# Kernel tuning notes

Measured on AMD Instinct MI355X. Metric: run time of the kernel, lower is better.

## Reference

```python
import jax, jax.numpy as jnp
import numpy as np

EMBED_DIM = 1024
NUM_HEADS = 16
HEAD_DIM = EMBED_DIM // NUM_HEADS
SCALE = 1.0 / np.sqrt(HEAD_DIM).astype(np.float32)


def setup_inputs() -> dict:
    key = jax.random.key(0)
    ks = jax.random.split(key, 9)
    B, T, C = 2, 2048, EMBED_DIM
    s = 1.0 / np.sqrt(C).astype(np.float32)  # torch Linear init scale (approx, uniform bound)
    return {
        "x_q": jax.random.normal(ks[0], (B, T, C), dtype=jnp.float32),
        "attn_mask": jnp.zeros((T, T), dtype=jnp.float32),
        "Wq": jax.random.uniform(ks[1], (C, C), jnp.float32, -s, s),
        "bq": jax.random.uniform(ks[2], (C,), jnp.float32, -s, s),
        "Wk": jax.random.uniform(ks[3], (C, C), jnp.float32, -s, s),
        "bk": jax.random.uniform(ks[4], (C,), jnp.float32, -s, s),
        "Wv": jax.random.uniform(ks[5], (C, C), jnp.float32, -s, s),
        "bv": jax.random.uniform(ks[6], (C,), jnp.float32, -s, s),
        "Wo": jax.random.uniform(ks[7], (C, C), jnp.float32, -s, s),
        "bo": jax.random.uniform(ks[8], (C,), jnp.float32, -s, s),
    }


def reference(x_q, attn_mask, Wq, bq, Wk, bk, Wv, bv, Wo, bo):
    B, Tq, C = x_q.shape
    # self-attention: x_kv = x_q
    q = (x_q @ Wq.T + bq).reshape(B, Tq, NUM_HEADS, HEAD_DIM)
    k = (x_q @ Wk.T + bk).reshape(B, Tq, NUM_HEADS, HEAD_DIM)
    v = (x_q @ Wv.T + bv).reshape(B, Tq, NUM_HEADS, HEAD_DIM)
    # (B, H, Tq, Tk)
    scores = jnp.einsum('bqhd,bkhd->bhqk', q, k) * SCALE
    scores = scores + attn_mask[None, None, :, :]  # 2D additive mask path
    attn = jax.nn.softmax(scores, axis=-1)  # dropout p=0.0 -> identity
    out = jnp.einsum('bhqk,bkhd->bqhd', attn, v).reshape(B, Tq, C)
    out = out @ Wo.T + bo
    return out
```

## Files before the change

kernel.cpp:

```cpp
#include <hip/hip_runtime.h>
#include <hip/hip_bf16.h>
#include <stdint.h>

typedef _Float16 f16x8_t __attribute__((ext_vector_type(8)));
typedef _Float16 f16x4_t __attribute__((ext_vector_type(4)));
typedef float    f32x4_t __attribute__((ext_vector_type(4)));

#define T_SEQ 2048
#define NH    16
#define HD    64
#define CDIM  1024
#define NTOK  4096
#define QSCALE 0.18033688011112042f
#define LOG2E  1.4426950408889634f

__device__ __forceinline__ void async_ld16(void* lds, const void* g) {
    __builtin_amdgcn_global_load_lds(
        (const __attribute__((address_space(1))) uint32_t*)g,
        (__attribute__((address_space(3))) uint32_t*)lds, 16, 0, 0);
}

__global__ __launch_bounds__(256)
void prep_all(const float* __restrict__ x, const float* __restrict__ Wq,
              const float* __restrict__ Wk, const float* __restrict__ Wv,
              const float* __restrict__ Wo, const float* __restrict__ mask,
              _Float16* __restrict__ xh, _Float16* __restrict__ Wqkvh,
              _Float16* __restrict__ Woh, int* __restrict__ flag)
{
    const int XQ = NTOK * CDIM / 4;
    const int WQ = CDIM * CDIM / 4;
    int i = blockIdx.x * 256 + threadIdx.x;
    if (i < XQ + 4 * WQ) {
        const float* s; _Float16* d; int off;
        if (i < XQ) { s = x; d = xh; off = i; }
        else {
            int j = i - XQ; int w = j >> 18; off = j & (WQ - 1);
            s = (w == 0) ? Wq : (w == 1) ? Wk : (w == 2) ? Wv : Wo;
            d = (w == 3) ? Woh : Wqkvh + (size_t)w * CDIM * CDIM;
        }
        float4 v = ((const float4*)s)[off];
        f16x4_t h = {(_Float16)v.x, (_Float16)v.y, (_Float16)v.z, (_Float16)v.w};
        ((f16x4_t*)d)[off] = h;
    } else {
        int off = i - (XQ + 4 * WQ);
        float4 v = ((const float4*)mask)[off];
        if (v.x != 0.f || v.y != 0.f || v.z != 0.f || v.w != 0.f) atomicOr(flag, 1);
    }
}

template<int MODE>
__global__ __launch_bounds__(256)
void gemm_f16(const _Float16* __restrict__ Ag, const _Float16* __restrict__ Bg,
              const float* __restrict__ b0, const float* __restrict__ b1,
              const float* __restrict__ b2,
              _Float16* __restrict__ Qo, _Float16* __restrict__ Ko,
              _Float16* __restrict__ Vto, float* __restrict__ Fo)
{
    __shared__ _Float16 sA[3][128 * 32];
    __shared__ _Float16 sB[3][128 * 32];
    const int K = CDIM;
    const int tid  = threadIdx.x;
    const int lane = tid & 63, wv = tid >> 6;
    const int wr = wv >> 1, wc = wv & 1;
    const int bid = blockIdx.x;
    const int xcd = bid & 7, L = bid >> 3;
    const int sb = L & 31, st = L >> 5;
    const int rowA0 = (st * 8 + (sb & 7)) * 128;
    const int rowB0 = (xcd * 4 + (sb >> 3)) * 128;
    const int srow = lane >> 2;
    const int scol = (((lane & 3) ^ (srow & 3)) * 8);
    const int fr = lane & 15, fg = lane >> 4;
    const int rsw = (fg ^ (fr & 3)) * 8;
    f32x4_t acc[4][4] = {};

#define STAGE(buf, kk) do {                                                     \
        _Pragma("unroll")                                                       \
        for (int i_ = 0; i_ < 2; ++i_) {                                        \
            const int eoff = i_ * 2048 + wv * 512;                              \
            const int r_ = i_ * 64 + wv * 16 + srow;                            \
            async_ld16(&sA[buf][eoff], Ag + (size_t)(rowA0 + r_) * K + (kk) + scol); \
            async_ld16(&sB[buf][eoff], Bg + (size_t)(rowB0 + r_) * K + (kk) + scol); \
        } } while (0)

    STAGE(0, 0);
    int cur = 0;
    for (int k0 = 0; k0 < K; k0 += 32) {
        const int nxt = (cur == 2) ? 0 : cur + 1;
        if (k0 + 32 < K) {
            STAGE(nxt, k0 + 32);
            asm volatile("s_waitcnt vmcnt(4)" ::: "memory");
        } else {
            asm volatile("s_waitcnt vmcnt(0)" ::: "memory");
        }
        __builtin_amdgcn_s_barrier();
        __builtin_amdgcn_sched_barrier(0);
        f16x8_t a[4], b[4];
#pragma unroll
        for (int mi = 0; mi < 4; ++mi)
            a[mi] = *(const f16x8_t*)&sA[cur][(wr * 64 + mi * 16 + fr) * 32 + rsw];
#pragma unroll
        for (int ni = 0; ni < 4; ++ni)
            b[ni] = *(const f16x8_t*)&sB[cur][(wc * 64 + ni * 16 + fr) * 32 + rsw];
#pragma unroll
        for (int mi = 0; mi < 4; ++mi)
#pragma unroll
            for (int ni = 0; ni < 4; ++ni)
                acc[mi][ni] = __builtin_amdgcn_mfma_f32_16x16x32_f16(a[mi], b[ni], acc[mi][ni], 0, 0, 0);
        cur = nxt;
    }
#undef STAGE

    if (MODE == 0) {
        const int which = rowA0 >> 10;
        const float* bp = (which == 0) ? b0 : ((which == 1) ? b1 : b2);
#pragma unroll
        for (int mi = 0; mi < 4; ++mi) {
            const int cc = (rowA0 & 1023) + wr * 64 + mi * 16 + fg * 4;
            const float4 bv = *(const float4*)&bp[cc];
            const int h = cc >> 6, d0 = cc & 63;
#pragma unroll
            for (int ni = 0; ni < 4; ++ni) {
                const int tok = rowB0 + wc * 64 + ni * 16 + fr;
                const int bh = (tok >> 11) * NH + h, tt = tok & (T_SEQ - 1);
                const float v0 = acc[mi][ni][0] + bv.x, v1 = acc[mi][ni][1] + bv.y;
                const float v2 = acc[mi][ni][2] + bv.z, v3 = acc[mi][ni][3] + bv.w;
                if (which == 0) {
                    f16x4_t hq = {(_Float16)(v0 * QSCALE), (_Float16)(v1 * QSCALE),
                                  (_Float16)(v2 * QSCALE), (_Float16)(v3 * QSCALE)};
                    *(f16x4_t*)&Qo[((size_t)bh * T_SEQ + tt) * HD + d0] = hq;
                } else if (which == 1) {
                    f16x4_t hk = {(_Float16)v0, (_Float16)v1, (_Float16)v2, (_Float16)v3};
                    *(f16x4_t*)&Ko[((size_t)bh * 32 + (tt >> 6)) * 4096 +
                                   (d0 >> 3) * 512 + (tt & 63) * 8 + (d0 & 7)] = hk;
                } else {
                    const size_t vb_ = ((size_t)bh * 32 + (tt >> 6)) * 4096 +
                                       (size_t)((tt >> 3) & 7) * 512 + (tt & 7);
                    Vto[vb_ + (d0 + 0) * 8] = (_Float16)v0;
                    Vto[vb_ + (d0 + 1) * 8] = (_Float16)v1;
                    Vto[vb_ + (d0 + 2) * 8] = (_Float16)v2;
                    Vto[vb_ + (d0 + 3) * 8] = (_Float16)v3;
                }
            }
        }
    } else {
#pragma unroll
        for (int mi = 0; mi < 4; ++mi) {
            const int cc = rowA0 + wr * 64 + mi * 16 + fg * 4;
            const float4 bv = *(const float4*)&b0[cc];
#pragma unroll
            for (int ni = 0; ni < 4; ++ni) {
                const int tok = rowB0 + wc * 64 + ni * 16 + fr;
                float4 ov = {acc[mi][ni][0] + bv.x, acc[mi][ni][1] + bv.y,
                             acc[mi][ni][2] + bv.z, acc[mi][ni][3] + bv.w};
                *(float4*)&Fo[(size_t)tok * CDIM + cc] = ov;
            }
        }
    }
}

__global__ __launch_bounds__(512, 4)
void attn_f16(const _Float16* __restrict__ Q, const _Float16* __restrict__ Kc,
              const _Float16* __restrict__ Vc, const float* __restrict__ mask,
              const int* __restrict__ mflag, _Float16* __restrict__ AO)
{
    __shared__ __align__(16) _Float16 sK[3][4096];
    __shared__ __align__(16) _Float16 sV[3][4096];

    const int tid = threadIdx.x;
    const int lane = tid & 63, wv = tid >> 6;
    const int fr = lane & 15, fg = lane >> 4;
    const int bid = blockIdx.x;
    const int swz = (bid & 7) * 64 + (bid >> 3);
    const int qx = swz & 15, bh = swz >> 4;
    const int b = bh >> 4, h = bh & (NH - 1);
    const int q0 = qx * 128 + wv * 16;
    const _Float16* Qb  = Q  + (size_t)bh * T_SEQ * HD;
    const _Float16* Kbh = Kc + (size_t)bh * (T_SEQ * HD);
    const _Float16* Vbh = Vc + (size_t)bh * (T_SEQ * HD);
    const int soff = wv * 512 + lane * 8;

    f16x8_t qf[2];
#pragma unroll
    for (int dc = 0; dc < 2; ++dc)
        qf[dc] = *(const f16x8_t*)&Qb[(size_t)(q0 + fr) * HD + dc * 32 + fg * 8];

    const f16x8_t ones = {(_Float16)1.f, (_Float16)1.f, (_Float16)1.f, (_Float16)1.f,
                          (_Float16)1.f, (_Float16)1.f, (_Float16)1.f, (_Float16)1.f};
    f32x4_t o[4] = {};
    f32x4_t lacc = {};
    float m_run = -1e30f;
    const int mf = mflag[0];

    async_ld16(&sK[0][wv * 512], Kbh + soff);
    async_ld16(&sV[0][wv * 512], Vbh + soff);
    int cur = 0;

    for (int t = 0; t < T_SEQ / 64; ++t) {
        const int nxt = (cur == 2) ? 0 : cur + 1;
        if (t + 1 < T_SEQ / 64) {
            async_ld16(&sK[nxt][wv * 512], Kbh + (size_t)(t + 1) * 4096 + soff);
            async_ld16(&sV[nxt][wv * 512], Vbh + (size_t)(t + 1) * 4096 + soff);
            asm volatile("s_waitcnt vmcnt(2)" ::: "memory");
        } else {
            asm volatile("s_waitcnt vmcnt(0)" ::: "memory");
        }
        __builtin_amdgcn_s_barrier();
        __builtin_amdgcn_sched_barrier(0);

        f32x4_t s[4];
        __builtin_amdgcn_s_setprio(1);
#pragma unroll
        for (int kt = 0; kt < 4; ++kt) {
            f16x8_t kf0 = *(const f16x8_t*)&sK[cur][fg * 512       + (kt * 16 + fr) * 8];
            f16x8_t kf1 = *(const f16x8_t*)&sK[cur][(4 + fg) * 512 + (kt * 16 + fr) * 8];
            f32x4_t z = {};
            z     = __builtin_amdgcn_mfma_f32_16x16x32_f16(kf0, qf[0], z, 0, 0, 0);
            s[kt] = __builtin_amdgcn_mfma_f32_16x16x32_f16(kf1, qf[1], z, 0, 0, 0);
        }
        __builtin_amdgcn_s_setprio(0);

        f16x8_t vb[2][4];
#pragma unroll
        for (int kt2 = 0; kt2 < 2; ++kt2)
#pragma unroll
            for (int df = 0; df < 4; ++df)
                vb[kt2][df] = *(const f16x8_t*)&sV[cur][(kt2 * 4 + fg) * 512 + (df * 16 + fr) * 8];

        if (mf) {
            const float* mrow = mask + (size_t)(q0 + fr) * T_SEQ + t * 64;
#pragma unroll
            for (int kt = 0; kt < 4; ++kt)
#pragma unroll
                for (int r = 0; r < 4; ++r)
                    s[kt][r] += mrow[kt * 16 + fg * 4 + r] * LOG2E;
        }

        const float t0 = fmaxf(fmaxf(s[0][0], s[0][1]), s[0][2]);
        const float t1 = fmaxf(fmaxf(s[0][3], s[1][0]), s[1][1]);
        const float t2 = fmaxf(fmaxf(s[1][2], s[1][3]), s[2][0]);
        const float t3 = fmaxf(fmaxf(s[2][1], s[2][2]), s[2][3]);
        const float t4 = fmaxf(fmaxf(s[3][0], s[3][1]), s[3][2]);
        float tmax = fmaxf(fmaxf(fmaxf(t0, t1), fmaxf(t2, t3)), fmaxf(t4, s[3][3]));
        tmax = fmaxf(tmax, __shfl_xor(tmax, 16, 64));
        tmax = fmaxf(tmax, __shfl_xor(tmax, 32, 64));

        if (!__all(tmax <= m_run + 8.0f)) {
            const float mnew = fmaxf(m_run, tmax);
            const float sc = __builtin_amdgcn_exp2f(m_run - mnew);
            m_run = mnew;
            float scq[4];
#pragma unroll
            for (int r = 0; r < 4; ++r)
                scq[r] = __shfl(sc, fg * 4 + r, 64);
#pragma unroll
            for (int r = 0; r < 4; ++r) {
                lacc[r] *= scq[r];
#pragma unroll
                for (int df = 0; df < 4; ++df)
                    o[df][r] *= scq[r];
            }
        }

        uint32_t U[4][2];
#pragma unroll
        for (int kt = 0; kt < 4; ++kt) {
            const float p0 = __builtin_amdgcn_exp2f(s[kt][0] - m_run);
            const float p1 = __builtin_amdgcn_exp2f(s[kt][1] - m_run);
            const float p2 = __builtin_amdgcn_exp2f(s[kt][2] - m_run);
            const float p3 = __builtin_amdgcn_exp2f(s[kt][3] - m_run);
            auto w0 = __builtin_amdgcn_cvt_pkrtz(p0, p1);
            auto w1 = __builtin_amdgcn_cvt_pkrtz(p2, p3);
            U[kt][0] = __builtin_bit_cast(uint32_t, w0);
            U[kt][1] = __builtin_bit_cast(uint32_t, w1);
        }

        f16x8_t pa[2];
#pragma unroll
        for (int kt2 = 0; kt2 < 2; ++kt2) {
            uint32_t w0, w1, w2, w3;
            {
                uint32_t y = U[2 * kt2][0], x = U[2 * kt2 + 1][0];
                asm("v_permlane32_swap_b32 %0, %1" : "+v"(y), "+v"(x));
                asm("v_permlane16_swap_b32 %0, %1" : "+v"(y), "+v"(x));
                w0 = y; w2 = x;
            }
            {
                uint32_t y = U[2 * kt2][1], x = U[2 * kt2 + 1][1];
                asm("v_permlane32_swap_b32 %0, %1" : "+v"(y), "+v"(x));
                asm("v_permlane16_swap_b32 %0, %1" : "+v"(y), "+v"(x));
                w1 = y; w3 = x;
            }
            union { uint32_t u4[4]; f16x8_t v; } uu;
            uu.u4[0] = w0; uu.u4[1] = w1; uu.u4[2] = w2; uu.u4[3] = w3;
            pa[kt2] = uu.v;
        }

        __builtin_amdgcn_s_setprio(1);
#pragma unroll
        for (int kt2 = 0; kt2 < 2; ++kt2) {
#pragma unroll
            for (int df = 0; df < 4; ++df)
                o[df] = __builtin_amdgcn_mfma_f32_16x16x32_f16(pa[kt2], vb[kt2][df], o[df], 0, 0, 0);
            lacc = __builtin_amdgcn_mfma_f32_16x16x32_f16(pa[kt2], ones, lacc, 0, 0, 0);
        }
        __builtin_amdgcn_s_setprio(0);
        cur = nxt;
    }

#pragma unroll
    for (int r = 0; r < 4; ++r) {
        const float inv = 1.f / lacc[r];
        const size_t row = (size_t)(b * T_SEQ + q0 + fg * 4 + r);
#pragma unroll
        for (int df = 0; df < 4; ++df)
            AO[row * CDIM + h * HD + df * 16 + fr] = (_Float16)(o[df][r] * inv);
    }
}

extern "C" void kernel_launch(void* const* d_in, const int* in_sizes, int n_in,
                              void* d_out, int out_size, void* d_ws, size_t ws_size,
                              hipStream_t stream) {
    const float* x    = (const float*)d_in[0];
    const float* mask = (const float*)d_in[1];
    const float* Wq   = (const float*)d_in[2];
    const float* bq   = (const float*)d_in[3];
    const float* Wk   = (const float*)d_in[4];
    const float* bk   = (const float*)d_in[5];
    const float* Wv   = (const float*)d_in[6];
    const float* bv   = (const float*)d_in[7];
    const float* Wo   = (const float*)d_in[8];
    const float* bo   = (const float*)d_in[9];
    float* out = (float*)d_out;

    char* ws = (char*)d_ws;
    _Float16* xh    = (_Float16*)(ws);
    _Float16* Wqkvh = (_Float16*)(ws + (8u  << 20));
    _Float16* Woh   = (_Float16*)(ws + (14u << 20));
    _Float16* Qp    = (_Float16*)(ws + (16u << 20));
    _Float16* Kc    = (_Float16*)(ws + (24u << 20));
    _Float16* Vc    = (_Float16*)(ws + (32u << 20));
    int* mflag      = (int*)(ws + (40u << 20));
    _Float16* AO    = xh;

    hipMemsetAsync(mflag, 0, 4, stream);
    prep_all<<<12288, 256, 0, stream>>>(x, Wq, Wk, Wv, Wo, mask, xh, Wqkvh, Woh, mflag);
    gemm_f16<0><<<768, 256, 0, stream>>>(Wqkvh, xh, bq, bk, bv, Qp, Kc, Vc, nullptr);
    attn_f16<<<512, 512, 0, stream>>>(Qp, Kc, Vc, mask, mflag, AO);
    gemm_f16<1><<<256, 256, 0, stream>>>(Woh, AO, bo, nullptr, nullptr,
                                         nullptr, nullptr, nullptr, out);
}
```

Baseline: 125.5 us.

## Use 256x256 tiled QKV GEMM with 8 waves and double-buffered K=64 stages

Replaces the 128x128-tile QKV projection GEMM (768 blocks of 256 threads) with a dedicated 256x256-tile kernel using 512 threads, K-step of 64, XOR-swizzled LDS, and double buffering. Next-stage async loads are interleaved between MFMA groups, and s_setprio raises priority around the MFMAs. This raises arithmetic intensity and cuts global/LDS traffic per FLOP. In exchange, only 192 blocks are launched on a 256-CU part, which under-fills the GPU and uses large LDS and register footprints. The output GEMM is split into its own non-templated kernel.

```diff
diff --git a/kernel.cpp b/kernel.cpp
--- a/kernel.cpp
+++ b/kernel.cpp
@@ -48,13 +48,129 @@
     }
 }
 
-template<int MODE>
+__global__ __launch_bounds__(512, 2)
+void gemm_qkv256(const _Float16* __restrict__ Ag, const _Float16* __restrict__ Bg,
+                 const float* __restrict__ b0, const float* __restrict__ b1,
+                 const float* __restrict__ b2,
+                 _Float16* __restrict__ Qo, _Float16* __restrict__ Ko,
+                 _Float16* __restrict__ Vto)
+{
+    __shared__ _Float16 sA[4][8192];
+    __shared__ _Float16 sB[4][8192];
+    const int K = CDIM;
+    const int tid  = threadIdx.x;
+    const int lane = tid & 63, wv = tid >> 6;
+    const int wr = wv >> 2, wc = wv & 3;
+    const int fr = lane & 15, fg = lane >> 4;
+    const int bid = blockIdx.x;
+    const int xcd = bid & 7, L = bid >> 3;
+    const int a_blk = L % 12, b_blk = xcd * 2 + (L / 12);
+    const int rowA0 = a_blk * 256, rowB0 = b_blk * 256;
+    const int t8 = tid & 7, trow = tid >> 3;
+    f32x4_t acc[8][4] = {};
+
+#define STHT(ptr, blk0, half, ktv, db, sh) do {                                      \
+        _Pragma("unroll")                                                            \
+        for (int j_ = 0; j_ < 2; ++j_) {                                             \
+            const int r_ = trow + j_ * 64;                                           \
+            const int sc_ = t8 ^ (r_ & 7);                                           \
+            async_ld16(&sh[(db) * 2 + (half)][j_ * 4096 + tid * 8],                  \
+                       ptr + (size_t)((blk0) + (half) * 128 + r_) * K + (ktv) * 64 + sc_ * 8); \
+        } } while (0)
+
+    STHT(Ag, rowA0, 0, 0, 0, sA);
+    STHT(Ag, rowA0, 1, 0, 0, sA);
+    STHT(Bg, rowB0, 0, 0, 0, sB);
+    STHT(Bg, rowB0, 1, 0, 0, sB);
+
+    const int NKT = K / 64;
+    for (int kt = 0; kt < NKT; ++kt) {
+        const int db = kt & 1;
+        __builtin_amdgcn_s_barrier();
+        if (kt + 1 < NKT) {
+            STHT(Ag, rowA0, 0, kt + 1, db ^ 1, sA);
+            asm volatile("s_waitcnt vmcnt(2)" ::: "memory");
+        } else {
+            asm volatile("s_waitcnt vmcnt(0)" ::: "memory");
+        }
+        __builtin_amdgcn_s_barrier();
+        __builtin_amdgcn_sched_barrier(0);
+
+        f16x8_t b[4][2];
+#pragma unroll
+        for (int ni = 0; ni < 4; ++ni)
+#pragma unroll
+            for (int ks = 0; ks < 2; ++ks) {
+                const int rowin = ((wc & 1) * 64) + ni * 16 + fr;
+                const int ch = (ks * 4 + fg) ^ (rowin & 7);
+                b[ni][ks] = *(const f16x8_t*)&sB[db * 2 + (wc >> 1)][rowin * 64 + ch * 8];
+            }
+#pragma unroll
+        for (int q = 0; q < 4; ++q) {
+            if (kt + 1 < NKT) {
+                if (q == 1)      STHT(Ag, rowA0, 1, kt + 1, db ^ 1, sA);
+                else if (q == 2) STHT(Bg, rowB0, 0, kt + 1, db ^ 1, sB);
+                else if (q == 3) STHT(Bg, rowB0, 1, kt + 1, db ^ 1, sB);
+            }
+            f16x8_t a[2][2];
+#pragma unroll
+            for (int m2 = 0; m2 < 2; ++m2)
+#pragma unroll
+                for (int ks = 0; ks < 2; ++ks) {
+                    const int rowin = (2 * q + m2) * 16 + fr;
+                    const int ch = (ks * 4 + fg) ^ (rowin & 7);
+                    a[m2][ks] = *(const f16x8_t*)&sA[db * 2 + wr][rowin * 64 + ch * 8];
+                }
+            __builtin_amdgcn_s_setprio(1);
+#pragma unroll
+            for (int m2 = 0; m2 < 2; ++m2)
+#pragma unroll
+                for (int ni = 0; ni < 4; ++ni)
+#pragma unroll
+                    for (int ks = 0; ks < 2; ++ks)
+                        acc[2 * q + m2][ni] = __builtin_amdgcn_mfma_f32_16x16x32_f16(
+                            a[m2][ks], b[ni][ks], acc[2 * q + m2][ni], 0, 0, 0);
+            __builtin_amdgcn_s_setprio(0);
+        }
+    }
+#undef STHT
+
+    const int which = a_blk >> 2;
+    const float* bp = (which == 0) ? b0 : ((which == 1) ? b1 : b2);
+#pragma unroll
+    for (int mi = 0; mi < 8; ++mi) {
+        const int cc = (rowA0 & 1023) + wr * 128 + mi * 16 + fg * 4;
+        const float4 bv = *(const float4*)&bp[cc];
+        const int h = cc >> 6, d0 = cc & 63;
+#pragma unroll
+        for (int ni = 0; ni < 4; ++ni) {
+            const int tok = rowB0 + wc * 64 + ni * 16 + fr;
+            const int bh = (tok >> 11) * NH + h, tt = tok & (T_SEQ - 1);
+            const float v0 = acc[mi][ni][0] + bv.x, v1 = acc[mi][ni][1] + bv.y;
+            const float v2 = acc[mi][ni][2] + bv.z, v3 = acc[mi][ni][3] + bv.w;
+            if (which == 0) {
+                f16x4_t hq = {(_Float16)(v0 * QSCALE), (_Float16)(v1 * QSCALE),
+                              (_Float16)(v2 * QSCALE), (_Float16)(v3 * QSCALE)};
+                *(f16x4_t*)&Qo[((size_t)bh * T_SEQ + tt) * HD + d0] = hq;
+            } else if (which == 1) {
+                f16x4_t hk = {(_Float16)v0, (_Float16)v1, (_Float16)v2, (_Float16)v3};
+                *(f16x4_t*)&Ko[((size_t)bh * 32 + (tt >> 6)) * 4096 +
+                               (d0 >> 3) * 512 + (tt & 63) * 8 + (d0 & 7)] = hk;
+            } else {
+                const size_t vb_ = ((size_t)bh * 32 + (tt >> 6)) * 4096 +
+                                   (size_t)((tt >> 3) & 7) * 512 + (tt & 7);
+                Vto[vb_ + (d0 + 0) * 8] = (_Float16)v0;
+                Vto[vb_ + (d0 + 1) * 8] = (_Float16)v1;
+                Vto[vb_ + (d0 + 2) * 8] = (_Float16)v2;
+                Vto[vb_ + (d0 + 3) * 8] = (_Float16)v3;
+            }
+        }
+    }
+}
+
 __global__ __launch_bounds__(256)
-void gemm_f16(const _Float16* __restrict__ Ag, const _Float16* __restrict__ Bg,
-              const float* __restrict__ b0, const float* __restrict__ b1,
-              const float* __restrict__ b2,
-              _Float16* __restrict__ Qo, _Float16* __restrict__ Ko,
-              _Float16* __restrict__ Vto, float* __restrict__ Fo)
+void gemm_out(const _Float16* __restrict__ Ag, const _Float16* __restrict__ Bg,
+              const float* __restrict__ b0, float* __restrict__ Fo)
 {
     __shared__ _Float16 sA[3][128 * 32];
     __shared__ _Float16 sB[3][128 * 32];
@@ -110,50 +226,16 @@
     }
 #undef STAGE
 
-    if (MODE == 0) {
-        const int which = rowA0 >> 10;
-        const float* bp = (which == 0) ? b0 : ((which == 1) ? b1 : b2);
-#pragma unroll
-        for (int mi = 0; mi < 4; ++mi) {
-            const int cc = (rowA0 & 1023) + wr * 64 + mi * 16 + fg * 4;
-            const float4 bv = *(const float4*)&bp[cc];
-            const int h = cc >> 6, d0 = cc & 63;
-#pragma unroll
-            for (int ni = 0; ni < 4; ++ni) {
-                const int tok = rowB0 + wc * 64 + ni * 16 + fr;
-                const int bh = (tok >> 11) * NH + h, tt = tok & (T_SEQ - 1);
-                const float v0 = acc[mi][ni][0] + bv.x, v1 = acc[mi][ni][1] + bv.y;
-                const float v2 = acc[mi][ni][2] + bv.z, v3 = acc[mi][ni][3] + bv.w;
-                if (which == 0) {
-                    f16x4_t hq = {(_Float16)(v0 * QSCALE), (_Float16)(v1 * QSCALE),
-                                  (_Float16)(v2 * QSCALE), (_Float16)(v3 * QSCALE)};
-                    *(f16x4_t*)&Qo[((size_t)bh * T_SEQ + tt) * HD + d0] = hq;
-                } else if (which == 1) {
-                    f16x4_t hk = {(_Float16)v0, (_Float16)v1, (_Float16)v2, (_Float16)v3};
-                    *(f16x4_t*)&Ko[((size_t)bh * 32 + (tt >> 6)) * 4096 +
-                                   (d0 >> 3) * 512 + (tt & 63) * 8 + (d0 & 7)] = hk;
-                } else {
-                    const size_t vb_ = ((size_t)bh * 32 + (tt >> 6)) * 4096 +
-                                       (size_t)((tt >> 3) & 7) * 512 + (tt & 7);
-                    Vto[vb_ + (d0 + 0) * 8] = (_Float16)v0;
-                    Vto[vb_ + (d0 + 1) * 8] = (_Float16)v1;
-                    Vto[vb_ + (d0 + 2) * 8] = (_Float16)v2;
-                    Vto[vb_ + (d0 + 3) * 8] = (_Float16)v3;
-                }
-            }
-        }
-    } else {
-#pragma unroll
-        for (int mi = 0; mi < 4; ++mi) {
-            const int cc = rowA0 + wr * 64 + mi * 16 + fg * 4;
-            const float4 bv = *(const float4*)&b0[cc];
-#pragma unroll
-            for (int ni = 0; ni < 4; ++ni) {
-                const int tok = rowB0 + wc * 64 + ni * 16 + fr;
-                float4 ov = {acc[mi][ni][0] + bv.x, acc[mi][ni][1] + bv.y,
-                             acc[mi][ni][2] + bv.z, acc[mi][ni][3] + bv.w};
-                *(float4*)&Fo[(size_t)tok * CDIM + cc] = ov;
-            }
+#pragma unroll
+    for (int mi = 0; mi < 4; ++mi) {
+        const int cc = rowA0 + wr * 64 + mi * 16 + fg * 4;
+        const float4 bv = *(const float4*)&b0[cc];
+#pragma unroll
+        for (int ni = 0; ni < 4; ++ni) {
+            const int tok = rowB0 + wc * 64 + ni * 16 + fr;
+            float4 ov = {acc[mi][ni][0] + bv.x, acc[mi][ni][1] + bv.y,
+                         acc[mi][ni][2] + bv.z, acc[mi][ni][3] + bv.w};
+            *(float4*)&Fo[(size_t)tok * CDIM + cc] = ov;
         }
     }
 }
@@ -344,8 +426,7 @@
 
     hipMemsetAsync(mflag, 0, 4, stream);
     prep_all<<<12288, 256, 0, stream>>>(x, Wq, Wk, Wv, Wo, mask, xh, Wqkvh, Woh, mflag);
-    gemm_f16<0><<<768, 256, 0, stream>>>(Wqkvh, xh, bq, bk, bv, Qp, Kc, Vc, nullptr);
+    gemm_qkv256<<<192, 512, 0, stream>>>(Wqkvh, xh, bq, bk, bv, Qp, Kc, Vc);
     attn_f16<<<512, 512, 0, stream>>>(Qp, Kc, Vc, mask, mflag, AO);
-    gemm_f16<1><<<256, 256, 0, stream>>>(Woh, AO, bo, nullptr, nullptr,
-                                         nullptr, nullptr, nullptr, out);
-}
+    gemm_out<<<256, 256, 0, stream>>>(Woh, AO, bo, out);
+}
```

Result: slower. 134.5 us (+7.2%).
